# Optimization experiments

Measured on AMD Instinct MI355X. Metric: run time of the kernel, lower is better.

Reference implementation:

```python
import jax, jax.numpy as jnp
import numpy as np

B, S, H, D, K = 262144, 120, 256, 64, 64  # batch, state_dim, vae_hidden_dim, latent_dim, n_codes


def _lin(k, i, o):
    return jax.random.normal(k, (i, o), jnp.float32) / np.sqrt(i).astype(np.float32)


def setup_inputs() -> dict:
    key = jax.random.key(0)
    ks = jax.random.split(key, 9)
    return {
        "inputs": jax.random.normal(ks[0], (B, S), jnp.float32),
        "enc_w1": _lin(ks[1], S, H), "enc_b1": jnp.zeros((H,), jnp.float32),
        "enc_w2": _lin(ks[2], H, H), "enc_b2": jnp.zeros((H,), jnp.float32),
        "enc_w3": _lin(ks[3], H, D), "enc_b3": jnp.zeros((D,), jnp.float32),
        "codebook": jax.random.uniform(ks[4], (K, D), jnp.float32),  # NearestEmbed weight (rand init)
        "fc3_w": _lin(ks[5], D, H), "fc3_b": jnp.zeros((H,), jnp.float32),
        "fc4_w": _lin(ks[6], H, H), "fc4_b": jnp.zeros((H,), jnp.float32),
        "fc5_w": _lin(ks[7], H, S), "fc5_b": jnp.zeros((S,), jnp.float32),
    }


def _nearest(z, codebook):
    # squared L2 distance via |z|^2 - 2 z.C^T + |c|^2; fused GEMM form
    d = ((z * z).sum(-1, keepdims=True)
         - 2.0 * (z @ codebook.T)
         + (codebook * codebook).sum(-1))  # [B, K]
    idx = jnp.argmin(d, axis=-1)  # [B]
    return codebook[idx], idx


def reference(inputs, enc_w1, enc_b1, enc_w2, enc_b2, enc_w3, enc_b3,
              codebook, fc3_w, fc3_b, fc4_w, fc4_b, fc5_w, fc5_b):
    # encode
    h = jax.nn.relu(inputs @ enc_w1 + enc_b1)
    h = jax.nn.relu(h @ enc_w2 + enc_b2)
    z_e = h @ enc_w3 + enc_b3  # [B, D]
    # emb(z_e, weight_sg=True): straight-through to input, codebook detached
    q, argmin = _nearest(z_e, jax.lax.stop_gradient(codebook))
    z_q = z_e + jax.lax.stop_gradient(q - z_e)
    # emb(z_e.detach()): grads flow only to codebook
    emb, _ = _nearest(jax.lax.stop_gradient(z_e), codebook)
    # decode (recon_type=1)
    r = jax.nn.relu(z_q @ fc3_w + fc3_b)
    r = jax.nn.relu(r @ fc4_w + fc4_b)
    s_hat = r @ fc5_w + fc5_b  # [B, S]
    return s_hat, z_e, emb, argmin
```

## Files before the change

kernel.cpp:

```cpp
#include <hip/hip_runtime.h>


#define B_TOTAL 262144
#define THR 0.02f

typedef float  f32x4 __attribute__((ext_vector_type(4)));
typedef short  s16x8 __attribute__((ext_vector_type(8)));

#define ZB ((size_t)B_TOTAL * 120)
#define EB ((size_t)B_TOTAL * 184)
#define AB ((size_t)B_TOTAL * 248)

#define WS_STAB   0
#define WS_CBT    30720
#define WS_CNORM  47104
#define WS_COUNT  47360
#define WS_LIST   47424
#define WS_PKW1   1096064
#define WS_PKW2   1227136
#define WS_PKE3   1489280
#define WS_PKCB   1554816

static __device__ __forceinline__ unsigned short f2bf(float x) {
    unsigned int u = __float_as_uint(x);
    return (unsigned short)((u + 0x7fffu + ((u >> 16) & 1u)) >> 16);
}
static __device__ __forceinline__ void splitbf(float a, unsigned short& h, unsigned short& s) {
    unsigned hb = __float_as_uint(a) & 0xffff0000u;
    h = (unsigned short)(hb >> 16);
    s = f2bf(a - __uint_as_float(hb));
}
static __device__ __forceinline__ float sqnc(float v) {
    float s = v * v;
    asm volatile("" : "+v"(s));
    return s;
}
static __device__ __forceinline__ float np_sumsq64(const float* a) {
    float r8[8];
#pragma unroll
    for (int j = 0; j < 8; ++j) r8[j] = sqnc(a[j]);
#pragma unroll
    for (int i = 8; i < 64; i += 8)
#pragma unroll
        for (int j = 0; j < 8; ++j) r8[j] += sqnc(a[i + j]);
    return ((r8[0] + r8[1]) + (r8[2] + r8[3])) + ((r8[4] + r8[5]) + (r8[6] + r8[7]));
}

static __device__ __forceinline__ int swz(int row, int col) {
    return row * 256 + ((((col >> 3) ^ (row & 7))) << 3) + (col & 7);
}

__global__ __launch_bounds__(256)
void vq_prep(const float* __restrict__ cb,
             const float* __restrict__ dw3, const float* __restrict__ db3,
             const float* __restrict__ dw4, const float* __restrict__ db4,
             const float* __restrict__ dw5, const float* __restrict__ db5,
             float* __restrict__ s_tab, float* __restrict__ cbT, float* __restrict__ cnorm)
{
    __shared__ float c_row[64];
    __shared__ float u1[256];
    __shared__ float u2[256];
    const int k = blockIdx.x;
    const int t = threadIdx.x;

    if (t < 64) c_row[t] = cb[k * 64 + t];
    __syncthreads();
    {
        float s = 0.f;
        for (int f = 0; f < 64; ++f) s = fmaf(c_row[f], dw3[f * 256 + t], s);
        u1[t] = fmaxf(s + db3[t], 0.f);
    }
    if (t < 64) cbT[t * 64 + k] = c_row[t];
    if (t == 0) cnorm[k] = np_sumsq64(&cb[k * 64]);
    __syncthreads();
    {
        float s = 0.f;
        for (int f = 0; f < 256; ++f) s = fmaf(u1[f], dw4[f * 256 + t], s);
        u2[t] = fmaxf(s + db4[t], 0.f);
    }
    __syncthreads();
    if (t < 120) {
        float o = 0.f;
        for (int f = 0; f < 256; ++f) o = fmaf(u2[f], dw5[f * 120 + t], o);
        s_tab[k * 120 + t] = o + db5[t];
    }
}

__global__ __launch_bounds__(512)
void vq_pack(const float* __restrict__ w1, const float* __restrict__ w2,
             const float* __restrict__ ew3, const float* __restrict__ cbT,
             unsigned short* __restrict__ pw1, unsigned short* __restrict__ pw2,
             unsigned short* __restrict__ pe3, unsigned short* __restrict__ pcb,
             int* __restrict__ flag_count)
{
    const int t = threadIdx.x;
    int f = blockIdx.x;
    if (f == 0 && t == 0) *flag_count = 0;

    const float* src; unsigned short* dst;
    int KSN, nt, ks, srcK, ld;
    if (f < 64)       { src = w1;  dst = pw1; KSN = 4; nt = f >> 2;  ks = f & 3; srcK = 120; ld = 256; }
    else if (f < 192) { f -= 64;  src = w2;  dst = pw2; KSN = 8; nt = f >> 3; ks = f & 7; srcK = 256; ld = 256; }
    else if (f < 224) { f -= 192; src = ew3; dst = pe3; KSN = 8; nt = f >> 3; ks = f & 7; srcK = 256; ld = 64; }
    else              { f -= 224; src = cbT; dst = pcb; KSN = 2; nt = f >> 1; ks = f & 1; srcK = 64;  ld = 64; }

    const int lane = t >> 3, j = t & 7;
    const int k = ks * 32 + (lane >> 4) * 8 + j;
    const int n = nt * 16 + (lane & 15);
    float a = (k < srcK) ? src[k * ld + n] : 0.f;
    unsigned short h, l;
    splitbf(a, h, l);
    const int base = (nt * KSN + ks) * 2 * 512;
    dst[base + t] = h;
    dst[base + 512 + t] = l;
}

__global__ __launch_bounds__(256, 4)
void vq_fast(const float* __restrict__ x,
             const float* __restrict__ b1, const float* __restrict__ b2,
             const float* __restrict__ eb3, const float* __restrict__ cb,
             const float* __restrict__ s_tab, const float* __restrict__ cnorm,
             const unsigned short* __restrict__ pw1, const unsigned short* __restrict__ pw2,
             const unsigned short* __restrict__ pe3, const unsigned short* __restrict__ pcb,
             int* __restrict__ flag_count, int* __restrict__ flag_list,
             float* __restrict__ out)
{
    __shared__ __align__(16) unsigned char smem[32768];
    unsigned short* ph = (unsigned short*)smem;
    unsigned short* pl = (unsigned short*)(smem + 16384);
    unsigned short* zh = (unsigned short*)smem;
    unsigned short* zl = (unsigned short*)(smem + 4608);
    float*          dm = (float*)(smem + 9216);
    int*          idxs = (int*)(smem + 17920);

    const int t = threadIdx.x;
    const int w = t >> 6, l = t & 63;
    const int lr = l & 15;
    const int grow0 = blockIdx.x * 32;

    {
        const float* xb = x + (size_t)grow0 * 120;
        unsigned* ph32 = (unsigned*)ph;
        unsigned* pl32 = (unsigned*)pl;
#pragma unroll
        for (int i = 0; i < 8; ++i) {
            int p = t + 256 * i;
            if (p < 1920) {
                int row = p / 60, c2 = p - row * 60;
                float2 v = *(const float2*)&xb[row * 120 + c2 * 2];
                unsigned short h0, l0, h1, l1;
                splitbf(v.x, h0, l0); splitbf(v.y, h1, l1);
                int o32 = row * 128 + ((((c2 >> 2) ^ (row & 7))) << 2) + (c2 & 3);
                ph32[o32] = (unsigned)h0 | ((unsigned)h1 << 16);
                pl32[o32] = (unsigned)l0 | ((unsigned)l1 << 16);
            }
        }
        if (t < 128) {
            int row = t >> 2, c2 = 60 + (t & 3);
            int o32 = row * 128 + ((((c2 >> 2) ^ (row & 7))) << 2) + (c2 & 3);
            ph32[o32] = 0u;
            pl32[o32] = 0u;
        }
    }
    __syncthreads();

    const int cbase = w * 64;

    {
        f32x4 acc[2][4];
#pragma unroll
        for (int a = 0; a < 2; ++a)
#pragma unroll
            for (int b = 0; b < 4; ++b) acc[a][b] = (f32x4)0.f;

#pragma unroll
        for (int ks = 0; ks < 4; ++ks) {
            const int kb = ks * 32 + (l >> 4) * 8;
            s16x8 ah[2], al[2], bh[4], bl[4];
#pragma unroll
            for (int rt = 0; rt < 2; ++rt) {
                const int ro = swz(rt * 16 + lr, kb);
                ah[rt] = *(const s16x8*)&ph[ro];
                al[rt] = *(const s16x8*)&pl[ro];
            }
#pragma unroll
            for (int ct = 0; ct < 4; ++ct) {
                const unsigned short* pb = pw1 + ((w * 4 + ct) * 4 + ks) * 2 * 512 + l * 8;
                bh[ct] = *(const s16x8*)pb;
                bl[ct] = *(const s16x8*)(pb + 512);
            }
            __builtin_amdgcn_s_setprio(1);
#pragma unroll
            for (int rt = 0; rt < 2; ++rt)
#pragma unroll
                for (int ct = 0; ct < 4; ++ct) {
                    acc[rt][ct] = __builtin_amdgcn_mfma_f32_16x16x32_bf16(ah[rt], bh[ct], acc[rt][ct], 0, 0, 0);
                    acc[rt][ct] = __builtin_amdgcn_mfma_f32_16x16x32_bf16(ah[rt], bl[ct], acc[rt][ct], 0, 0, 0);
                    acc[rt][ct] = __builtin_amdgcn_mfma_f32_16x16x32_bf16(al[rt], bh[ct], acc[rt][ct], 0, 0, 0);
                }
            __builtin_amdgcn_s_setprio(0);
        }
        __syncthreads();
#pragma unroll
        for (int ct = 0; ct < 4; ++ct) {
            const int col = cbase + ct * 16 + lr;
            const float bb = b1[col];
#pragma unroll
            for (int rt = 0; rt < 2; ++rt)
#pragma unroll
                for (int r = 0; r < 4; ++r) {
                    float v = fmaxf(acc[rt][ct][r] + bb, 0.f);
                    unsigned short h, s;
                    splitbf(v, h, s);
                    const int row = rt * 16 + (l >> 4) * 4 + r;
                    const int o = swz(row, col);
                    ph[o] = h;
                    pl[o] = s;
                }
        }
    }
    __syncthreads();

    {
        f32x4 acc[2][4];
#pragma unroll
        for (int a = 0; a < 2; ++a)
#pragma unroll
            for (int b = 0; b < 4; ++b) acc[a][b] = (f32x4)0.f;

#pragma unroll
        for (int ks = 0; ks < 8; ++ks) {
            const int kb = ks * 32 + (l >> 4) * 8;
            s16x8 ah[2], al[2], bh[4], bl[4];
#pragma unroll
            for (int rt = 0; rt < 2; ++rt) {
                const int ro = swz(rt * 16 + lr, kb);
                ah[rt] = *(const s16x8*)&ph[ro];
                al[rt] = *(const s16x8*)&pl[ro];
            }
#pragma unroll
            for (int ct = 0; ct < 4; ++ct) {
                const unsigned short* pb = pw2 + ((w * 4 + ct) * 8 + ks) * 2 * 512 + l * 8;
                bh[ct] = *(const s16x8*)pb;
                bl[ct] = *(const s16x8*)(pb + 512);
            }
            __builtin_amdgcn_s_setprio(1);
#pragma unroll
            for (int rt = 0; rt < 2; ++rt)
#pragma unroll
                for (int ct = 0; ct < 4; ++ct) {
                    acc[rt][ct] = __builtin_amdgcn_mfma_f32_16x16x32_bf16(ah[rt], bh[ct], acc[rt][ct], 0, 0, 0);
                    acc[rt][ct] = __builtin_amdgcn_mfma_f32_16x16x32_bf16(ah[rt], bl[ct], acc[rt][ct], 0, 0, 0);
                    acc[rt][ct] = __builtin_amdgcn_mfma_f32_16x16x32_bf16(al[rt], bh[ct], acc[rt][ct], 0, 0, 0);
                }
            __builtin_amdgcn_s_setprio(0);
        }
        __syncthreads();
#pragma unroll
        for (int ct = 0; ct < 4; ++ct) {
            const int col = cbase + ct * 16 + lr;
            const float bb = b2[col];
#pragma unroll
            for (int rt = 0; rt < 2; ++rt)
#pragma unroll
                for (int r = 0; r < 4; ++r) {
                    float v = fmaxf(acc[rt][ct][r] + bb, 0.f);
                    unsigned short h, s;
                    splitbf(v, h, s);
                    const int row = rt * 16 + (l >> 4) * 4 + r;
                    const int o = swz(row, col);
                    ph[o] = h;
                    pl[o] = s;
                }
        }
    }
    __syncthreads();

    const int r3 = (w & 1) * 16;
    const int ch = w >> 1;
    {
        f32x4 a3[2];
#pragma unroll
        for (int b = 0; b < 2; ++b) a3[b] = (f32x4)0.f;

#pragma unroll
        for (int ks = 0; ks < 8; ++ks) {
            const int kb = ks * 32 + (l >> 4) * 8;
            const int ro = swz(r3 + lr, kb);
            s16x8 ah = *(const s16x8*)&ph[ro];
            s16x8 al = *(const s16x8*)&pl[ro];
#pragma unroll
            for (int ct = 0; ct < 2; ++ct) {
                const unsigned short* pb = pe3 + ((ch * 2 + ct) * 8 + ks) * 2 * 512 + l * 8;
                s16x8 bh = *(const s16x8*)pb;
                s16x8 bl = *(const s16x8*)(pb + 512);
                __builtin_amdgcn_s_setprio(1);
                a3[ct] = __builtin_amdgcn_mfma_f32_16x16x32_bf16(ah, bh, a3[ct], 0, 0, 0);
                a3[ct] = __builtin_amdgcn_mfma_f32_16x16x32_bf16(ah, bl, a3[ct], 0, 0, 0);
                a3[ct] = __builtin_amdgcn_mfma_f32_16x16x32_bf16(al, bh, a3[ct], 0, 0, 0);
                __builtin_amdgcn_s_setprio(0);
            }
        }
        __syncthreads();
#pragma unroll
        for (int ct = 0; ct < 2; ++ct) {
            const int col = ch * 32 + ct * 16 + lr;
            const float eb = eb3[col];
#pragma unroll
            for (int r = 0; r < 4; ++r) {
                const int row = r3 + (l >> 4) * 4 + r;
                float z = a3[ct][r] + eb;
                out[ZB + (size_t)(grow0 + row) * 64 + col] = z;
                unsigned short h, s;
                splitbf(z, h, s);
                zh[row * 72 + col] = h;
                zl[row * 72 + col] = s;
            }
        }
    }
    __syncthreads();

    {
        f32x4 a4[2];
#pragma unroll
        for (int b = 0; b < 2; ++b) a4[b] = (f32x4)0.f;
#pragma unroll
        for (int ks = 0; ks < 2; ++ks) {
            const int kb = ks * 32 + (l >> 4) * 8;
            const int ro = (r3 + lr) * 72 + kb;
            s16x8 ah = *(const s16x8*)&zh[ro];
            s16x8 al = *(const s16x8*)&zl[ro];
#pragma unroll
            for (int ct = 0; ct < 2; ++ct) {
                const unsigned short* pb = pcb + ((ch * 2 + ct) * 2 + ks) * 2 * 512 + l * 8;
                s16x8 bh = *(const s16x8*)pb;
                s16x8 bl = *(const s16x8*)(pb + 512);
                __builtin_amdgcn_s_setprio(1);
                a4[ct] = __builtin_amdgcn_mfma_f32_16x16x32_bf16(ah, bh, a4[ct], 0, 0, 0);
                a4[ct] = __builtin_amdgcn_mfma_f32_16x16x32_bf16(ah, bl, a4[ct], 0, 0, 0);
                a4[ct] = __builtin_amdgcn_mfma_f32_16x16x32_bf16(al, bh, a4[ct], 0, 0, 0);
                __builtin_amdgcn_s_setprio(0);
            }
        }
#pragma unroll
        for (int ct = 0; ct < 2; ++ct) {
            const int col = ch * 32 + ct * 16 + lr;
            const float cn = cnorm[col];
#pragma unroll
            for (int r = 0; r < 4; ++r) {
                const int row = r3 + (l >> 4) * 4 + r;
                dm[row * 68 + col] = cn - 2.f * a4[ct][r];
            }
        }
    }
    __syncthreads();

    if (t < 32) {
        const float* dr = dm + t * 68;
        float best = dr[0], sec = 3.4e38f;
        int bi = 0;
        for (int j = 1; j < 64; ++j) {
            float v = dr[j];
            if (v < best) { sec = best; best = v; bi = j; }
            else if (v < sec) sec = v;
        }
        idxs[t] = bi;
        out[AB + grow0 + t] = (float)bi;
        if (sec - best < THR) {
            int p = atomicAdd(flag_count, 1);
            if (p < B_TOTAL) flag_list[p] = grow0 + t;
        }
    }
    __syncthreads();

#pragma unroll
    for (int i = 0; i < 8; ++i) {
        int p = t + 256 * i;
        int row = p >> 6, c = p & 63;
        out[EB + (size_t)blockIdx.x * 2048 + p] = cb[idxs[row] * 64 + c];
    }
#pragma unroll
    for (int i = 0; i < 15; ++i) {
        int p = t + 256 * i;
        int row = p / 120, c = p - row * 120;
        out[(size_t)blockIdx.x * 3840 + p] = s_tab[idxs[row] * 120 + c];
    }
}

__global__ __launch_bounds__(256)
void vq_exact(const float* __restrict__ x,
              const float* __restrict__ w1, const float* __restrict__ b1,
              const float* __restrict__ w2, const float* __restrict__ b2,
              const float* __restrict__ ew3, const float* __restrict__ eb3,
              const float* __restrict__ cb,
              const float* __restrict__ s_tab,
              const float* __restrict__ cbT, const float* __restrict__ cnorm,
              const int* __restrict__ flag_count, const int* __restrict__ flag_list,
              float* __restrict__ out)
{
    __shared__ float act[256 * 18];
    __shared__ float zrm[16 * 68];
    __shared__ float dmr[16 * 68];
    __shared__ float A_lds[16];
    __shared__ int   idxs[16];
    __shared__ int   rl[16];

    const int t = threadIdx.x;
    int count = *flag_count;
    if (count > B_TOTAL) count = B_TOTAL;

    const int tx = t & 31;
    const int ty = t >> 5;
    const int r0 = ty * 2;
    const int c0 = tx * 8;
    const int c0d = tx * 2;

    for (int base = blockIdx.x * 16; base < count; base += 1024 * 16) {
        if (t < 16) {
            int li = base + t;
            rl[t] = flag_list[li < count ? li : count - 1];
        }
        __syncthreads();

        for (int i = 0; i < 8; ++i) {
            int p = t + 256 * i;
            if (p < 1920) {
                int r = p / 120;
                int c = p - r * 120;
                act[c * 18 + r] = x[(size_t)rl[r] * 120 + c];
            }
        }
        __syncthreads();

        {
            float acc[2][8];
#pragma unroll
            for (int i = 0; i < 2; ++i)
#pragma unroll
                for (int c = 0; c < 8; ++c) acc[i][c] = 0.f;
#pragma unroll 2
            for (int k = 0; k < 120; ++k) {
                const float2 av = *(const float2*)&act[k * 18 + r0];
                const float4 wv0 = *(const float4*)&w1[k * 256 + c0];
                const float4 wv1 = *(const float4*)&w1[k * 256 + c0 + 4];
                const float a[2] = {av.x, av.y};
                const float wv[8] = {wv0.x, wv0.y, wv0.z, wv0.w, wv1.x, wv1.y, wv1.z, wv1.w};
#pragma unroll
                for (int i = 0; i < 2; ++i)
#pragma unroll
                    for (int c = 0; c < 8; ++c) acc[i][c] = fmaf(a[i], wv[c], acc[i][c]);
            }
            __syncthreads();
            const float4 bv0 = *(const float4*)&b1[c0];
            const float4 bv1 = *(const float4*)&b1[c0 + 4];
            const float bb[8] = {bv0.x, bv0.y, bv0.z, bv0.w, bv1.x, bv1.y, bv1.z, bv1.w};
#pragma unroll
            for (int c = 0; c < 8; ++c)
#pragma unroll
                for (int i = 0; i < 2; ++i)
                    act[(c0 + c) * 18 + r0 + i] = fmaxf(acc[i][c] + bb[c], 0.f);
        }
        __syncthreads();

        {
            float acc[2][8];
#pragma unroll
            for (int i = 0; i < 2; ++i)
#pragma unroll
                for (int c = 0; c < 8; ++c) acc[i][c] = 0.f;
#pragma unroll 2
            for (int k = 0; k < 256; ++k) {
                const float2 av = *(const float2*)&act[k * 18 + r0];
                const float4 wv0 = *(const float4*)&w2[k * 256 + c0];
                const float4 wv1 = *(const float4*)&w2[k * 256 + c0 + 4];
                const float a[2] = {av.x, av.y};
                const float wv[8] = {wv0.x, wv0.y, wv0.z, wv0.w, wv1.x, wv1.y, wv1.z, wv1.w};
#pragma unroll
                for (int i = 0; i < 2; ++i)
#pragma unroll
                    for (int c = 0; c < 8; ++c) acc[i][c] = fmaf(a[i], wv[c], acc[i][c]);
            }
            __syncthreads();
            const float4 bv0 = *(const float4*)&b2[c0];
            const float4 bv1 = *(const float4*)&b2[c0 + 4];
            const float bb[8] = {bv0.x, bv0.y, bv0.z, bv0.w, bv1.x, bv1.y, bv1.z, bv1.w};
#pragma unroll
            for (int c = 0; c < 8; ++c)
#pragma unroll
                for (int i = 0; i < 2; ++i)
                    act[(c0 + c) * 18 + r0 + i] = fmaxf(acc[i][c] + bb[c], 0.f);
        }
        __syncthreads();

        {
            float acc2[2][2];
#pragma unroll
            for (int i = 0; i < 2; ++i) { acc2[i][0] = 0.f; acc2[i][1] = 0.f; }
#pragma unroll 2
            for (int k = 0; k < 256; ++k) {
                const float2 av = *(const float2*)&act[k * 18 + r0];
                const float2 wv = *(const float2*)&ew3[k * 64 + c0d];
#pragma unroll
                for (int i = 0; i < 2; ++i) {
                    float a = (i == 0) ? av.x : av.y;
                    acc2[i][0] = fmaf(a, wv.x, acc2[i][0]);
                    acc2[i][1] = fmaf(a, wv.y, acc2[i][1]);
                }
            }
            __syncthreads();
            const float2 bv = *(const float2*)&eb3[c0d];
#pragma unroll
            for (int i = 0; i < 2; ++i) {
                float z0 = acc2[i][0] + bv.x;
                float z1 = acc2[i][1] + bv.y;
                act[(c0d + 0) * 18 + r0 + i] = z0;
                act[(c0d + 1) * 18 + r0 + i] = z1;
                zrm[(r0 + i) * 68 + c0d]     = z0;
                zrm[(r0 + i) * 68 + c0d + 1] = z1;
            }
        }
        __syncthreads();

        if (t < 16) A_lds[t] = np_sumsq64(&zrm[t * 68]);
        __syncthreads();

        {
            float acc3[2][2];
#pragma unroll
            for (int i = 0; i < 2; ++i) { acc3[i][0] = 0.f; acc3[i][1] = 0.f; }
#pragma unroll 2
            for (int k = 0; k < 64; ++k) {
                const float2 av = *(const float2*)&act[k * 18 + r0];
                const float2 wv = *(const float2*)&cbT[k * 64 + c0d];
#pragma unroll
                for (int i = 0; i < 2; ++i) {
                    float a = (i == 0) ? av.x : av.y;
                    acc3[i][0] = fmaf(a, wv.x, acc3[i][0]);
                    acc3[i][1] = fmaf(a, wv.y, acc3[i][1]);
                }
            }
            const float cn0 = cnorm[c0d], cn1 = cnorm[c0d + 1];
#pragma unroll
            for (int i = 0; i < 2; ++i) {
                float g0 = 2.0f * acc3[i][0];  asm volatile("" : "+v"(g0));
                float g1 = 2.0f * acc3[i][1];  asm volatile("" : "+v"(g1));
                const float Ar = A_lds[r0 + i];
                dmr[(r0 + i) * 68 + c0d]     = (Ar - g0) + cn0;
                dmr[(r0 + i) * 68 + c0d + 1] = (Ar - g1) + cn1;
            }
        }
        __syncthreads();

        if (t < 16) {
            const float* dr = &dmr[t * 68];
            float best = dr[0];
            int bi = 0;
            for (int c = 1; c < 64; ++c) {
                float v = dr[c];
                if (v < best) { best = v; bi = c; }
            }
            idxs[t] = bi;
            out[AB + rl[t]] = (float)bi;
        }
        __syncthreads();

        {
            const int r = t >> 4, q = t & 15;
            *(float4*)(out + ZB + (size_t)rl[r] * 64 + q * 4) = *(const float4*)&zrm[r * 68 + q * 4];
        }
        {
            const int r = t >> 4, q = t & 15;
            *(float4*)(out + EB + (size_t)rl[r] * 64 + q * 4) = *(const float4*)(cb + idxs[r] * 64 + q * 4);
        }
        for (int i = 0; i < 8; ++i) {
            int p = t + 256 * i;
            if (p < 1920) {
                int r = p / 120;
                int c = p - r * 120;
                out[(size_t)rl[r] * 120 + c] = s_tab[idxs[r] * 120 + c];
            }
        }
        __syncthreads();
    }
}

extern "C" void kernel_launch(void* const* d_in, const int* in_sizes, int n_in,
                              void* d_out, int out_size, void* d_ws, size_t ws_size,
                              hipStream_t stream)
{
    const float* x   = (const float*)d_in[0];
    const float* w1  = (const float*)d_in[1];
    const float* b1  = (const float*)d_in[2];
    const float* w2  = (const float*)d_in[3];
    const float* b2  = (const float*)d_in[4];
    const float* ew3 = (const float*)d_in[5];
    const float* eb3 = (const float*)d_in[6];
    const float* cb  = (const float*)d_in[7];
    const float* dw3 = (const float*)d_in[8];
    const float* db3 = (const float*)d_in[9];
    const float* dw4 = (const float*)d_in[10];
    const float* db4 = (const float*)d_in[11];
    const float* dw5 = (const float*)d_in[12];
    const float* db5 = (const float*)d_in[13];

    float* out = (float*)d_out;
    char* ws = (char*)d_ws;
    float* s_tab = (float*)(ws + WS_STAB);
    float* cbT   = (float*)(ws + WS_CBT);
    float* cnorm = (float*)(ws + WS_CNORM);
    int*   fcnt  = (int*)(ws + WS_COUNT);
    int*   flist = (int*)(ws + WS_LIST);
    unsigned short* pw1 = (unsigned short*)(ws + WS_PKW1);
    unsigned short* pw2 = (unsigned short*)(ws + WS_PKW2);
    unsigned short* pe3 = (unsigned short*)(ws + WS_PKE3);
    unsigned short* pcb = (unsigned short*)(ws + WS_PKCB);

    vq_prep<<<64, 256, 0, stream>>>(cb, dw3, db3, dw4, db4, dw5, db5,
                                    s_tab, cbT, cnorm);
    vq_pack<<<232, 512, 0, stream>>>(w1, w2, ew3, cbT, pw1, pw2, pe3, pcb, fcnt);
    vq_fast<<<B_TOTAL / 32, 256, 0, stream>>>(x, b1, b2, eb3, cb, s_tab, cnorm,
                                              pw1, pw2, pe3, pcb, fcnt, flist, out);
    vq_exact<<<1024, 256, 0, stream>>>(x, w1, b1, w2, b2, ew3, eb3, cb,
                                       s_tab, cbT, cnorm, fcnt, flist, out);
}
```

Before: 513.6 us.

## Use 512 threads per block in vq_fast and truncate low bf16 split

The fast VQ kernel now runs 8 waves per 32-row block instead of 4. Each wave computes half as many output column tiles in the MLP GEMMs, and one 16x16 tile in the z and distance GEMMs. The bf16 hi/lo split now truncates the residual instead of rounding it, which saves a few ALU ops per element but loses a little precision. More waves per block should hide latency better, at the cost of more duplicated A-fragment LDS reads and more sync overhead.

```diff
diff --git a/kernel.cpp b/kernel.cpp
--- a/kernel.cpp
+++ b/kernel.cpp
@@ -29,6 +29,12 @@
     unsigned hb = __float_as_uint(a) & 0xffff0000u;
     h = (unsigned short)(hb >> 16);
     s = f2bf(a - __uint_as_float(hb));
+}
+static __device__ __forceinline__ void splitbf_t(float a, unsigned short& h, unsigned short& s) {
+    unsigned u = __float_as_uint(a);
+    h = (unsigned short)(u >> 16);
+    float d = a - __uint_as_float(u & 0xffff0000u);
+    s = (unsigned short)(__float_as_uint(d) >> 16);
 }
 static __device__ __forceinline__ float sqnc(float v) {
     float s = v * v;
@@ -115,7 +121,7 @@
     dst[base + 512 + t] = l;
 }
 
-__global__ __launch_bounds__(256, 4)
+__global__ __launch_bounds__(512, 4)
 void vq_fast(const float* __restrict__ x,
              const float* __restrict__ b1, const float* __restrict__ b2,
              const float* __restrict__ eb3, const float* __restrict__ cb,
@@ -143,16 +149,20 @@
         unsigned* ph32 = (unsigned*)ph;
         unsigned* pl32 = (unsigned*)pl;
 #pragma unroll
-        for (int i = 0; i < 8; ++i) {
-            int p = t + 256 * i;
+        for (int i = 0; i < 4; ++i) {
+            int p = t + 512 * i;
             if (p < 1920) {
                 int row = p / 60, c2 = p - row * 60;
                 float2 v = *(const float2*)&xb[row * 120 + c2 * 2];
-                unsigned short h0, l0, h1, l1;
-                splitbf(v.x, h0, l0); splitbf(v.y, h1, l1);
+                unsigned u0 = __float_as_uint(v.x);
+                unsigned u1 = __float_as_uint(v.y);
+                unsigned h0u = u0 & 0xffff0000u;
+                unsigned h1u = u1 & 0xffff0000u;
+                float d0 = v.x - __uint_as_float(h0u);
+                float d1 = v.y - __uint_as_float(h1u);
                 int o32 = row * 128 + ((((c2 >> 2) ^ (row & 7))) << 2) + (c2 & 3);
-                ph32[o32] = (unsigned)h0 | ((unsigned)h1 << 16);
-                pl32[o32] = (unsigned)l0 | ((unsigned)l1 << 16);
+                ph32[o32] = (u0 >> 16) | h1u;
+                pl32[o32] = (__float_as_uint(d0) >> 16) | (__float_as_uint(d1) & 0xffff0000u);
             }
         }
         if (t < 128) {
@@ -164,36 +174,35 @@
     }
     __syncthreads();
 
-    const int cbase = w * 64;
-
     {
-        f32x4 acc[2][4];
+        f32x4 acc[2][2];
 #pragma unroll
         for (int a = 0; a < 2; ++a)
 #pragma unroll
-            for (int b = 0; b < 4; ++b) acc[a][b] = (f32x4)0.f;
+            for (int b = 0; b < 2; ++b) acc[a][b] = (f32x4)0.f;
 
 #pragma unroll
         for (int ks = 0; ks < 4; ++ks) {
             const int kb = ks * 32 + (l >> 4) * 8;
-            s16x8 ah[2], al[2], bh[4], bl[4];
+            s16x8 ah[2], al[2];
 #pragma unroll
             for (int rt = 0; rt < 2; ++rt) {
                 const int ro = swz(rt * 16 + lr, kb);
                 ah[rt] = *(const s16x8*)&ph[ro];
                 al[rt] = *(const s16x8*)&pl[ro];
             }
-#pragma unroll
-            for (int ct = 0; ct < 4; ++ct) {
-                const unsigned short* pb = pw1 + ((w * 4 + ct) * 4 + ks) * 2 * 512 + l * 8;
+            s16x8 bh[2], bl[2];
+#pragma unroll
+            for (int ct = 0; ct < 2; ++ct) {
+                const unsigned short* pb = pw1 + ((w * 2 + ct) * 4 + ks) * 1024 + l * 8;
                 bh[ct] = *(const s16x8*)pb;
                 bl[ct] = *(const s16x8*)(pb + 512);
             }
             __builtin_amdgcn_s_setprio(1);
 #pragma unroll
-            for (int rt = 0; rt < 2; ++rt)
-#pragma unroll
-                for (int ct = 0; ct < 4; ++ct) {
+            for (int ct = 0; ct < 2; ++ct)
+#pragma unroll
+                for (int rt = 0; rt < 2; ++rt) {
                     acc[rt][ct] = __builtin_amdgcn_mfma_f32_16x16x32_bf16(ah[rt], bh[ct], acc[rt][ct], 0, 0, 0);
                     acc[rt][ct] = __builtin_amdgcn_mfma_f32_16x16x32_bf16(ah[rt], bl[ct], acc[rt][ct], 0, 0, 0);
                     acc[rt][ct] = __builtin_amdgcn_mfma_f32_16x16x32_bf16(al[rt], bh[ct], acc[rt][ct], 0, 0, 0);
@@ -202,8 +211,8 @@
         }
         __syncthreads();
 #pragma unroll
-        for (int ct = 0; ct < 4; ++ct) {
-            const int col = cbase + ct * 16 + lr;
+        for (int ct = 0; ct < 2; ++ct) {
+            const int col = w * 32 + ct * 16 + lr;
             const float bb = b1[col];
 #pragma unroll
             for (int rt = 0; rt < 2; ++rt)
@@ -211,7 +220,7 @@
                 for (int r = 0; r < 4; ++r) {
                     float v = fmaxf(acc[rt][ct][r] + bb, 0.f);
                     unsigned short h, s;
-                    splitbf(v, h, s);
+                    splitbf_t(v, h, s);
                     const int row = rt * 16 + (l >> 4) * 4 + r;
                     const int o = swz(row, col);
                     ph[o] = h;
@@ -222,33 +231,34 @@
     __syncthreads();
 
     {
-        f32x4 acc[2][4];
+        f32x4 acc[2][2];
 #pragma unroll
         for (int a = 0; a < 2; ++a)
 #pragma unroll
-            for (int b = 0; b < 4; ++b) acc[a][b] = (f32x4)0.f;
+            for (int b = 0; b < 2; ++b) acc[a][b] = (f32x4)0.f;
 
 #pragma unroll
         for (int ks = 0; ks < 8; ++ks) {
             const int kb = ks * 32 + (l >> 4) * 8;
-            s16x8 ah[2], al[2], bh[4], bl[4];
+            s16x8 ah[2], al[2];
 #pragma unroll
             for (int rt = 0; rt < 2; ++rt) {
                 const int ro = swz(rt * 16 + lr, kb);
                 ah[rt] = *(const s16x8*)&ph[ro];
                 al[rt] = *(const s16x8*)&pl[ro];
             }
-#pragma unroll
-            for (int ct = 0; ct < 4; ++ct) {
-                const unsigned short* pb = pw2 + ((w * 4 + ct) * 8 + ks) * 2 * 512 + l * 8;
+            s16x8 bh[2], bl[2];
+#pragma unroll
+            for (int ct = 0; ct < 2; ++ct) {
+                const unsigned short* pb = pw2 + ((w * 2 + ct) * 8 + ks) * 1024 + l * 8;
                 bh[ct] = *(const s16x8*)pb;
                 bl[ct] = *(const s16x8*)(pb + 512);
             }
             __builtin_amdgcn_s_setprio(1);
 #pragma unroll
-            for (int rt = 0; rt < 2; ++rt)
-#pragma unroll
-                for (int ct = 0; ct < 4; ++ct) {
+            for (int ct = 0; ct < 2; ++ct)
+#pragma unroll
+                for (int rt = 0; rt < 2; ++rt) {
                     acc[rt][ct] = __builtin_amdgcn_mfma_f32_16x16x32_bf16(ah[rt], bh[ct], acc[rt][ct], 0, 0, 0);
                     acc[rt][ct] = __builtin_amdgcn_mfma_f32_16x16x32_bf16(ah[rt], bl[ct], acc[rt][ct], 0, 0, 0);
                     acc[rt][ct] = __builtin_amdgcn_mfma_f32_16x16x32_bf16(al[rt], bh[ct], acc[rt][ct], 0, 0, 0);
@@ -257,8 +267,8 @@
         }
         __syncthreads();
 #pragma unroll
-        for (int ct = 0; ct < 4; ++ct) {
-            const int col = cbase + ct * 16 + lr;
+        for (int ct = 0; ct < 2; ++ct) {
+            const int col = w * 32 + ct * 16 + lr;
             const float bb = b2[col];
 #pragma unroll
             for (int rt = 0; rt < 2; ++rt)
@@ -266,7 +276,7 @@
                 for (int r = 0; r < 4; ++r) {
                     float v = fmaxf(acc[rt][ct][r] + bb, 0.f);
                     unsigned short h, s;
-                    splitbf(v, h, s);
+                    splitbf_t(v, h, s);
                     const int row = rt * 16 + (l >> 4) * 4 + r;
                     const int o = swz(row, col);
                     ph[o] = h;
@@ -276,43 +286,37 @@
     }
     __syncthreads();
 
-    const int r3 = (w & 1) * 16;
-    const int ch = w >> 1;
+    const int rt3 = (w & 1) * 16;
+    const int ct3 = w >> 1;
     {
-        f32x4 a3[2];
-#pragma unroll
-        for (int b = 0; b < 2; ++b) a3[b] = (f32x4)0.f;
+        f32x4 a3 = (f32x4)0.f;
 
 #pragma unroll
         for (int ks = 0; ks < 8; ++ks) {
             const int kb = ks * 32 + (l >> 4) * 8;
-            const int ro = swz(r3 + lr, kb);
+            const int ro = swz(rt3 + lr, kb);
             s16x8 ah = *(const s16x8*)&ph[ro];
             s16x8 al = *(const s16x8*)&pl[ro];
-#pragma unroll
-            for (int ct = 0; ct < 2; ++ct) {
-                const unsigned short* pb = pe3 + ((ch * 2 + ct) * 8 + ks) * 2 * 512 + l * 8;
-                s16x8 bh = *(const s16x8*)pb;
-                s16x8 bl = *(const s16x8*)(pb + 512);
-                __builtin_amdgcn_s_setprio(1);
-                a3[ct] = __builtin_amdgcn_mfma_f32_16x16x32_bf16(ah, bh, a3[ct], 0, 0, 0);
-                a3[ct] = __builtin_amdgcn_mfma_f32_16x16x32_bf16(ah, bl, a3[ct], 0, 0, 0);
-                a3[ct] = __builtin_amdgcn_mfma_f32_16x16x32_bf16(al, bh, a3[ct], 0, 0, 0);
-                __builtin_amdgcn_s_setprio(0);
-            }
-        }
-        __syncthreads();
-#pragma unroll
-        for (int ct = 0; ct < 2; ++ct) {
-            const int col = ch * 32 + ct * 16 + lr;
+            const unsigned short* pb = pe3 + (ct3 * 8 + ks) * 1024 + l * 8;
+            s16x8 bh = *(const s16x8*)pb;
+            s16x8 bl = *(const s16x8*)(pb + 512);
+            __builtin_amdgcn_s_setprio(1);
+            a3 = __builtin_amdgcn_mfma_f32_16x16x32_bf16(ah, bh, a3, 0, 0, 0);
+            a3 = __builtin_amdgcn_mfma_f32_16x16x32_bf16(ah, bl, a3, 0, 0, 0);
+            a3 = __builtin_amdgcn_mfma_f32_16x16x32_bf16(al, bh, a3, 0, 0, 0);
+            __builtin_amdgcn_s_setprio(0);
+        }
+        __syncthreads();
+        {
+            const int col = ct3 * 16 + lr;
             const float eb = eb3[col];
 #pragma unroll
             for (int r = 0; r < 4; ++r) {
-                const int row = r3 + (l >> 4) * 4 + r;
-                float z = a3[ct][r] + eb;
+                const int row = rt3 + (l >> 4) * 4 + r;
+                float z = a3[r] + eb;
                 out[ZB + (size_t)(grow0 + row) * 64 + col] = z;
                 unsigned short h, s;
-                splitbf(z, h, s);
+                splitbf_t(z, h, s);
                 zh[row * 72 + col] = h;
                 zl[row * 72 + col] = s;
             }
@@ -321,35 +325,29 @@
     __syncthreads();
 
     {
-        f32x4 a4[2];
-#pragma unroll
-        for (int b = 0; b < 2; ++b) a4[b] = (f32x4)0.f;
+        f32x4 a4 = (f32x4)0.f;
 #pragma unroll
         for (int ks = 0; ks < 2; ++ks) {
             const int kb = ks * 32 + (l >> 4) * 8;
-            const int ro = (r3 + lr) * 72 + kb;
+            const int ro = (rt3 + lr) * 72 + kb;
             s16x8 ah = *(const s16x8*)&zh[ro];
             s16x8 al = *(const s16x8*)&zl[ro];
-#pragma unroll
-            for (int ct = 0; ct < 2; ++ct) {
-                const unsigned short* pb = pcb + ((ch * 2 + ct) * 2 + ks) * 2 * 512 + l * 8;
-                s16x8 bh = *(const s16x8*)pb;
-                s16x8 bl = *(const s16x8*)(pb + 512);
-                __builtin_amdgcn_s_setprio(1);
-                a4[ct] = __builtin_amdgcn_mfma_f32_16x16x32_bf16(ah, bh, a4[ct], 0, 0, 0);
-                a4[ct] = __builtin_amdgcn_mfma_f32_16x16x32_bf16(ah, bl, a4[ct], 0, 0, 0);
-                a4[ct] = __builtin_amdgcn_mfma_f32_16x16x32_bf16(al, bh, a4[ct], 0, 0, 0);
-                __builtin_amdgcn_s_setprio(0);
-            }
-        }
-#pragma unroll
-        for (int ct = 0; ct < 2; ++ct) {
-            const int col = ch * 32 + ct * 16 + lr;
+            const unsigned short* pb = pcb + (ct3 * 2 + ks) * 1024 + l * 8;
+            s16x8 bh = *(const s16x8*)pb;
+            s16x8 bl = *(const s16x8*)(pb + 512);
+            __builtin_amdgcn_s_setprio(1);
+            a4 = __builtin_amdgcn_mfma_f32_16x16x32_bf16(ah, bh, a4, 0, 0, 0);
+            a4 = __builtin_amdgcn_mfma_f32_16x16x32_bf16(ah, bl, a4, 0, 0, 0);
+            a4 = __builtin_amdgcn_mfma_f32_16x16x32_bf16(al, bh, a4, 0, 0, 0);
+            __builtin_amdgcn_s_setprio(0);
+        }
+        {
+            const int col = ct3 * 16 + lr;
             const float cn = cnorm[col];
 #pragma unroll
             for (int r = 0; r < 4; ++r) {
-                const int row = r3 + (l >> 4) * 4 + r;
-                dm[row * 68 + col] = cn - 2.f * a4[ct][r];
+                const int row = rt3 + (l >> 4) * 4 + r;
+                dm[row * 68 + col] = cn - 2.f * a4[r];
             }
         }
     }
@@ -374,16 +372,18 @@
     __syncthreads();
 
 #pragma unroll
-    for (int i = 0; i < 8; ++i) {
-        int p = t + 256 * i;
+    for (int i = 0; i < 4; ++i) {
+        int p = t + 512 * i;
         int row = p >> 6, c = p & 63;
         out[EB + (size_t)blockIdx.x * 2048 + p] = cb[idxs[row] * 64 + c];
     }
 #pragma unroll
-    for (int i = 0; i < 15; ++i) {
-        int p = t + 256 * i;
-        int row = p / 120, c = p - row * 120;
-        out[(size_t)blockIdx.x * 3840 + p] = s_tab[idxs[row] * 120 + c];
+    for (int i = 0; i < 8; ++i) {
+        int p = t + 512 * i;
+        if (p < 3840) {
+            int row = p / 120, c = p - row * 120;
+            out[(size_t)blockIdx.x * 3840 + p] = s_tab[idxs[row] * 120 + c];
+        }
     }
 }
 
@@ -618,7 +618,7 @@
     vq_prep<<<64, 256, 0, stream>>>(cb, dw3, db3, dw4, db4, dw5, db5,
                                     s_tab, cbT, cnorm);
     vq_pack<<<232, 512, 0, stream>>>(w1, w2, ew3, cbT, pw1, pw2, pe3, pcb, fcnt);
-    vq_fast<<<B_TOTAL / 32, 256, 0, stream>>>(x, b1, b2, eb3, cb, s_tab, cnorm,
+    vq_fast<<<B_TOTAL / 32, 512, 0, stream>>>(x, b1, b2, eb3, cb, s_tab, cnorm,
                                               pw1, pw2, pe3, pcb, fcnt, flist, out);
     vq_exact<<<1024, 256, 0, stream>>>(x, w1, b1, w2, b2, ew3, eb3, cb,
                                        s_tab, cbT, cnorm, fcnt, flist, out);
```

Measured after the change: 444.2 us. 1.16x faster.
